# Optimization experiments

Hardware: AMD Instinct MI355X
Metric: run time of the kernel (lower is better)

## Reference

```python
import jax, jax.numpy as jnp
import numpy as np

B, C, H, W = 4, 128, 64, 64


def setup_inputs() -> dict:
    key = jax.random.key(0)
    ks = jax.random.split(key, 7)
    s = 1.0 / np.sqrt(C)
    return {
        "x": jax.random.normal(ks[0], (B, C, H, W), dtype=jnp.float32),
        "Wq": jax.random.normal(ks[1], (C, C), dtype=jnp.float32) * s,
        "bq": jnp.zeros((C,), dtype=jnp.float32),
        "Wk": jax.random.normal(ks[2], (C, C), dtype=jnp.float32) * s,
        "bk": jnp.zeros((C,), dtype=jnp.float32),
        "Wv": jax.random.normal(ks[3], (C, C), dtype=jnp.float32) * s,
        "bv": jnp.zeros((C,), dtype=jnp.float32),
    }


def reference(x, Wq, bq, Wk, bk, Wv, bv):
    b, c, h, w = x.shape
    n = h * w
    scale = c ** (-0.5)
    # tokens: [B, N, C]
    xt = x.reshape(b, c, n).transpose(0, 2, 1)
    # 1x1 convs == per-token channel GEMMs (out[c'] = sum_c W[c',c] x[c] + b[c'])
    q = jnp.einsum("bnc,dc->bnd", xt, Wq) + bq  # [B, N, C]
    k = jnp.einsum("bnc,dc->bnd", xt, Wk) + bk  # [B, N, C]
    v = jnp.einsum("bnc,dc->bnd", xt, Wv) + bv  # [B, N, C]
    scores = jnp.einsum("bic,bjc->bij", q, k) * scale  # [B, N, N]
    attn = jax.nn.softmax(scores, axis=-1)
    out = jnp.einsum("bij,bjc->bic", attn, v)  # [B, N, C]
    return out.transpose(0, 2, 1).reshape(b, c, h, w)
```

## Files before the change

### kernel.cpp

```cpp
#include <hip/hip_runtime.h>
#include <hip/hip_bf16.h>


#define BATCH 4
#define CH    128
#define NTOK  4096
#define TK    64
#define SCALE 0.08838834764831845f
#define LOG2E 1.4426950408889634f
#define MFIX  16.0f

typedef __attribute__((ext_vector_type(8)))  short short8;
typedef __attribute__((ext_vector_type(4)))  float f32x4;
typedef __attribute__((ext_vector_type(16))) float f32x16;

static __device__ __forceinline__ unsigned short f2bf(float f) {
    __hip_bfloat16 h = (__hip_bfloat16)f;
    return *(const unsigned short*)&h;
}

static __device__ __forceinline__ unsigned cvt_pk_bf16(float lo, float hi) {
    unsigned r;
    asm("v_cvt_pk_bf16_f32 %0, %1, %2" : "=v"(r) : "v"(lo), "v"(hi));
    return r;
}

__global__ __launch_bounds__(256) void convert_w_kernel(
    const float* __restrict__ Wq, const float* __restrict__ Wk,
    const float* __restrict__ Wv, unsigned short* __restrict__ wb)
{
    const int idx = (blockIdx.x * 256 + threadIdx.x) * 4;
    const float* srcs[3] = {Wq, Wk, Wv};
    #pragma unroll
    for (int m = 0; m < 3; ++m) {
        float4 v = *(const float4*)(srcs[m] + idx);
        unsigned short o[4] = {f2bf(v.x), f2bf(v.y), f2bf(v.z), f2bf(v.w)};
        *(uint2*)(wb + (size_t)m * CH * CH + idx) = *(const uint2*)o;
    }
}

__global__ __launch_bounds__(256) void proj_mfma_kernel(
    const float* __restrict__ x,
    const unsigned short* __restrict__ wb_all,
    const float* __restrict__ bq, const float* __restrict__ bk,
    const float* __restrict__ bv,
    unsigned short* __restrict__ q_ws, unsigned short* __restrict__ k_ws,
    unsigned short* __restrict__ vt_ws)
{
    __shared__ __align__(16) unsigned short XsT[64 * CH];

    const int t    = threadIdx.x;
    const int w    = t >> 6;
    const int lane = t & 63;
    const int quad = lane >> 4;
    const int c16  = lane & 15;
    const int n0   = blockIdx.x * 64;
    const int b    = blockIdx.y;
    const int z    = blockIdx.z;
    const float* xb = x + (size_t)b * CH * NTOK;

    {
        const int tok = lane;
        #pragma unroll
        for (int cc = 0; cc < 4; ++cc) {
            const int cb = 32 * w + 8 * cc;
            unsigned short tmp[8];
            #pragma unroll
            for (int j = 0; j < 8; ++j)
                tmp[j] = f2bf(xb[(size_t)(cb + j) * NTOK + n0 + tok]);
            const int phys = ((cb >> 3) ^ (tok & 15));
            *(short8*)&XsT[tok * CH + phys * 8] = *(const short8*)tmp;
        }
    }
    __syncthreads();

    if (z < 2) {
        const unsigned short* wm = wb_all + (size_t)z * CH * CH;
        const float* bias = (z == 0) ? bq : bk;
        unsigned short* dst = (z == 0) ? q_ws : k_ws;
        const float mul = (z == 0) ? (SCALE * LOG2E) : 1.0f;

        short8 xa[4];
        #pragma unroll
        for (int ks = 0; ks < 4; ++ks)
            xa[ks] = *(const short8*)&XsT[(16 * w + c16) * CH + (((4 * ks + quad) ^ c16) << 3)];

        #pragma unroll
        for (int nt = 0; nt < 8; ++nt) {
            f32x4 a = (f32x4){0.f, 0.f, 0.f, 0.f};
            const unsigned short* wr = wm + (16 * nt + c16) * CH;
            #pragma unroll
            for (int ks = 0; ks < 4; ++ks) {
                const short8 bf = *(const short8*)(wr + 32 * ks + 8 * quad);
                a = __builtin_amdgcn_mfma_f32_16x16x32_bf16(xa[ks], bf, a, 0, 0, 0);
            }
            const float bvv = bias[16 * nt + c16];
            #pragma unroll
            for (int r = 0; r < 4; ++r) {
                const int n = n0 + 16 * w + quad * 4 + r;
                dst[((size_t)b * NTOK + n) * CH + 16 * nt + c16] =
                    f2bf((a[r] + bvv) * mul);
            }
        }
    } else {
        const unsigned short* wvb = wb_all + (size_t)2 * CH * CH;
        short8 wva[2][4];
        float  bvv[2][4];
        #pragma unroll
        for (int mt = 0; mt < 2; ++mt) {
            const int crow16 = 16 * (2 * w + mt);
            #pragma unroll
            for (int ks = 0; ks < 4; ++ks)
                wva[mt][ks] = *(const short8*)&wvb[(crow16 + c16) * CH + 32 * ks + 8 * quad];
            #pragma unroll
            for (int r = 0; r < 4; ++r)
                bvv[mt][r] = bv[crow16 + quad * 4 + r];
        }
        #pragma unroll
        for (int nt = 0; nt < 4; ++nt) {
            short8 xbf[4];
            #pragma unroll
            for (int ks = 0; ks < 4; ++ks)
                xbf[ks] = *(const short8*)&XsT[(16 * nt + c16) * CH + (((4 * ks + quad) ^ c16) << 3)];
            #pragma unroll
            for (int mt = 0; mt < 2; ++mt) {
                f32x4 acc = (f32x4){0.f, 0.f, 0.f, 0.f};
                #pragma unroll
                for (int ks = 0; ks < 4; ++ks)
                    acc = __builtin_amdgcn_mfma_f32_16x16x32_bf16(wva[mt][ks], xbf[ks], acc, 0, 0, 0);
                #pragma unroll
                for (int r = 0; r < 4; ++r) {
                    const int crow = 16 * (2 * w + mt) + quad * 4 + r;
                    vt_ws[((size_t)b * CH + crow) * NTOK + n0 + 16 * nt + c16] =
                        f2bf(acc[r] + bvv[mt][r]);
                }
            }
        }
    }
}

template <int SPLIT>
__global__ __launch_bounds__(256, 2) void flash_attn_mfma(
    const unsigned short* __restrict__ q_ws,
    const unsigned short* __restrict__ k_ws,
    const unsigned short* __restrict__ vt_ws,
    float* __restrict__ out,
    float* __restrict__ Op, float* __restrict__ l_p)
{
    __shared__ __align__(16) unsigned short KsU[2][TK * CH];
    __shared__ __align__(16) unsigned short VtU[2][CH * TK];

    const int t    = threadIdx.x;
    const int w    = t >> 6;
    const int lane = t & 63;
    const int half = lane >> 5;
    const int l32  = lane & 31;
    const int jc   = blockIdx.y;
    const int b    = blockIdx.z;
    const int n0   = blockIdx.x * 128;
    const int jbeg = jc * (NTOK / SPLIT);
    constexpr int NT = (NTOK / SPLIT) / TK;

    const unsigned short* kg = k_ws  + (size_t)b * NTOK * CH;
    const unsigned short* vg = vt_ws + (size_t)b * CH * NTOK;

    short8 qa[8];
    {
        const unsigned short* qrow =
            q_ws + ((size_t)b * NTOK + n0 + 32 * w + l32) * CH;
        #pragma unroll
        for (int ks = 0; ks < 8; ++ks)
            qa[ks] = *(const short8*)(qrow + ks * 16 + half * 8);
    }

    f32x16 Oa[4];
    #pragma unroll
    for (int ct = 0; ct < 4; ++ct) Oa[ct] = (f32x16)(0.0f);
    float lsum = 0.f;

    const int krl = lane >> 4, ku = lane & 15;
    const int vcl = lane >> 3, vu = lane & 7;

    auto STAGE = [&](int buf, int jj) {
        #pragma unroll
        for (int ci = 0; ci < 4; ++ci) {
            const int row = 16 * w + 4 * ci + krl;
            const int g   = ku ^ (row & 15);
            const unsigned short* src = kg + (size_t)(jj + row) * CH + g * 8;
            __builtin_amdgcn_global_load_lds(
                (const __attribute__((address_space(1))) void*)src,
                (__attribute__((address_space(3))) void*)&KsU[buf][(16 * w + 4 * ci) * CH],
                16, 0, 0);
        }
        #pragma unroll
        for (int ci = 0; ci < 4; ++ci) {
            const int c = 32 * w + 8 * ci + vcl;
            const int g = vu ^ (c & 7);
            const unsigned short* src = vg + (size_t)c * NTOK + jj + g * 8;
            __builtin_amdgcn_global_load_lds(
                (const __attribute__((address_space(1))) void*)src,
                (__attribute__((address_space(3))) void*)&VtU[buf][(32 * w + 8 * ci) * TK],
                16, 0, 0);
        }
    };

    STAGE(0, jbeg);

    int j0 = jbeg;
    for (int tt = 0; tt < NT; ++tt, j0 += TK) {
        const int cur = tt & 1;
        if (tt + 1 < NT) {
            STAGE(cur ^ 1, j0 + TK);
            asm volatile("s_waitcnt vmcnt(8)" ::: "memory");
        } else {
            asm volatile("s_waitcnt vmcnt(0)" ::: "memory");
        }
        __builtin_amdgcn_sched_barrier(0);
        __builtin_amdgcn_s_barrier();
        __builtin_amdgcn_sched_barrier(0);

        const unsigned short* Kc = &KsU[cur][0];
        const unsigned short* Vc = &VtU[cur][0];

        f32x16 s[2];
        s[0] = (f32x16)(-MFIX);
        s[1] = (f32x16)(-MFIX);
        #pragma unroll
        for (int ks = 0; ks < 8; ++ks) {
            const int ph = (2 * ks + half) ^ (l32 & 15);
            const short8 kf0 = *(const short8*)&Kc[l32 * CH + ph * 8];
            const short8 kf1 = *(const short8*)&Kc[(32 + l32) * CH + ph * 8];
            s[0] = __builtin_amdgcn_mfma_f32_32x32x16_bf16(kf0, qa[ks], s[0], 0, 0, 0);
            s[1] = __builtin_amdgcn_mfma_f32_32x32x16_bf16(kf1, qa[ks], s[1], 0, 0, 0);
        }

        short8 pb[4];
        #pragma unroll
        for (int kt = 0; kt < 2; ++kt) {
            float p[16];
            #pragma unroll
            for (int r = 0; r < 16; ++r) p[r] = exp2f(s[kt][r]);
            float a0 = 0.f, a1 = 0.f, a2 = 0.f, a3 = 0.f;
            #pragma unroll
            for (int r = 0; r < 4; ++r) {
                a0 += p[r]; a1 += p[4 + r]; a2 += p[8 + r]; a3 += p[12 + r];
            }
            lsum += (a0 + a1) + (a2 + a3);
            unsigned wd[8];
            #pragma unroll
            for (int i = 0; i < 8; ++i) wd[i] = cvt_pk_bf16(p[2 * i], p[2 * i + 1]);
            auto r02 = __builtin_amdgcn_permlane32_swap(wd[0], wd[2], false, false);
            auto r13 = __builtin_amdgcn_permlane32_swap(wd[1], wd[3], false, false);
            auto r46 = __builtin_amdgcn_permlane32_swap(wd[4], wd[6], false, false);
            auto r57 = __builtin_amdgcn_permlane32_swap(wd[5], wd[7], false, false);
            union { unsigned u[4]; short8 s8; } f0, f1;
            f0.u[0] = r02[0]; f0.u[1] = r13[0]; f0.u[2] = r02[1]; f0.u[3] = r13[1];
            f1.u[0] = r46[0]; f1.u[1] = r57[0]; f1.u[2] = r46[1]; f1.u[3] = r57[1];
            pb[2 * kt + 0] = f0.s8;
            pb[2 * kt + 1] = f1.s8;
        }

        #pragma unroll
        for (int ks2 = 0; ks2 < 4; ++ks2) {
            #pragma unroll
            for (int ct = 0; ct < 4; ++ct) {
                const int ch = 32 * ct + l32;
                const int ph = (2 * ks2 + half) ^ (ch & 7);
                const short8 vf = *(const short8*)&Vc[ch * TK + ph * 8];
                Oa[ct] = __builtin_amdgcn_mfma_f32_32x32x16_bf16(vf, pb[ks2], Oa[ct], 0, 0, 0);
            }
        }
        __builtin_amdgcn_sched_barrier(0);
        __builtin_amdgcn_s_barrier();
        __builtin_amdgcn_sched_barrier(0);
    }

    const float lt = lsum + __shfl_xor(lsum, 32);
    const int n = n0 + 32 * w + l32;

    if constexpr (SPLIT == 1) {
        const float inv = 1.0f / lt;
        #pragma unroll
        for (int ct = 0; ct < 4; ++ct) {
            #pragma unroll
            for (int r = 0; r < 16; ++r) {
                const int c = 32 * ct + (r & 3) + 8 * (r >> 2) + 4 * half;
                out[((size_t)b * CH + c) * NTOK + n] = Oa[ct][r] * inv;
            }
        }
    } else {
        const size_t chunk = (size_t)(b * SPLIT + jc);
        #pragma unroll
        for (int ct = 0; ct < 4; ++ct) {
            #pragma unroll
            for (int r = 0; r < 16; ++r) {
                const int c = 32 * ct + (r & 3) + 8 * (r >> 2) + 4 * half;
                Op[(chunk * CH + c) * NTOK + n] = Oa[ct][r];
            }
        }
        if (half == 0) l_p[chunk * NTOK + n] = lt;
    }
}

template <int SPLIT>
__global__ __launch_bounds__(256) void combine_kernel(
    const float* __restrict__ Op, const float* __restrict__ l_p,
    float* __restrict__ out)
{
    const int b = blockIdx.y;
    const size_t idx = ((size_t)blockIdx.x * 256 + threadIdx.x) * 4;
    const int c = (int)(idx >> 12);
    const int n = (int)(idx & (NTOK - 1));
    float4 acc = make_float4(0.f, 0.f, 0.f, 0.f);
    float4 den = make_float4(0.f, 0.f, 0.f, 0.f);
    #pragma unroll
    for (int j = 0; j < SPLIT; ++j) {
        const size_t chunk = (size_t)(b * SPLIT + j);
        const float4 o = *(const float4*)&Op[(chunk * CH + c) * NTOK + n];
        const float4 d = *(const float4*)&l_p[chunk * NTOK + n];
        acc.x += o.x; acc.y += o.y; acc.z += o.z; acc.w += o.w;
        den.x += d.x; den.y += d.y; den.z += d.z; den.w += d.w;
    }
    float4 r;
    r.x = acc.x / den.x; r.y = acc.y / den.y;
    r.z = acc.z / den.z; r.w = acc.w / den.w;
    *(float4*)&out[((size_t)b * CH * NTOK) + idx] = r;
}

extern "C" void kernel_launch(void* const* d_in, const int* in_sizes, int n_in,
                              void* d_out, int out_size, void* d_ws, size_t ws_size,
                              hipStream_t stream) {
    const float* x  = (const float*)d_in[0];
    const float* Wq = (const float*)d_in[1];
    const float* bq = (const float*)d_in[2];
    const float* Wk = (const float*)d_in[3];
    const float* bk = (const float*)d_in[4];
    const float* Wv = (const float*)d_in[5];
    const float* bv = (const float*)d_in[6];
    float* out = (float*)d_out;

    const size_t QKV = (size_t)BATCH * NTOK * CH;
    unsigned short* q_ws  = (unsigned short*)d_ws;
    unsigned short* k_ws  = q_ws + QKV;
    unsigned short* vt_ws = k_ws + QKV;
    unsigned short* wb    = vt_ws + QKV;
    float* Op = (float*)(wb + 3 * CH * CH);

    const size_t baseBytes = 3 * QKV * 2 + 3 * CH * CH * 2;
    auto needBytes = [&](size_t S) {
        return baseBytes + S * BATCH * NTOK * (size_t)(CH * 4 + 4);
    };

    convert_w_kernel<<<CH * CH / (256 * 4), 256, 0, stream>>>(Wq, Wk, Wv, wb);

    dim3 gp(NTOK / 64, BATCH, 3);
    proj_mfma_kernel<<<gp, 256, 0, stream>>>(x, wb, bq, bk, bv, q_ws, k_ws, vt_ws);

    dim3 gc(CH * NTOK / 1024, BATCH);
    if (ws_size >= needBytes(4)) {
        float* l_p = Op + (size_t)4 * BATCH * NTOK * CH;
        dim3 ga(NTOK / 128, 4, BATCH);
        flash_attn_mfma<4><<<ga, 256, 0, stream>>>(q_ws, k_ws, vt_ws, out, Op, l_p);
        combine_kernel<4><<<gc, 256, 0, stream>>>(Op, l_p, out);
    } else if (ws_size >= needBytes(2)) {
        float* l_p = Op + (size_t)2 * BATCH * NTOK * CH;
        dim3 ga(NTOK / 128, 2, BATCH);
        flash_attn_mfma<2><<<ga, 256, 0, stream>>>(q_ws, k_ws, vt_ws, out, Op, l_p);
        combine_kernel<2><<<gc, 256, 0, stream>>>(Op, l_p, out);
    } else {
        dim3 ga(NTOK / 128, 1, BATCH);
        flash_attn_mfma<1><<<ga, 256, 0, stream>>>(q_ws, k_ws, vt_ws, out,
                                                   nullptr, nullptr);
    }
}
```

Measured before the change: 132.1 us.

## Stage projection stores via LDS, register-stage V tiles, split attention 8-way

The projection kernel now writes its bf16 Q/K and V^T results into a padded shared-memory tile first, then issues coalesced 16-byte global stores instead of scattered 2-byte ones. In the flash-attention kernel, V is loaded into registers and written to a single shared buffer, while K keeps its double-buffered direct-to-LDS DMA. The loop is unrolled by two with explicit wait/barrier points, and launch bounds are raised to 3 blocks per CU now that LDS use is smaller. The host also prefers an 8-way key split when workspace allows, at the cost of more partial-output traffic in the combine step.

```diff
diff --git a/kernel.cpp b/kernel.cpp
--- a/kernel.cpp
+++ b/kernel.cpp
@@ -48,6 +48,7 @@
     unsigned short* __restrict__ vt_ws)
 {
     __shared__ __align__(16) unsigned short XsT[64 * CH];
+    __shared__ __align__(16) unsigned short Ep[128 * 72];
 
     const int t    = threadIdx.x;
     const int w    = t >> 6;
@@ -97,10 +98,17 @@
             const float bvv = bias[16 * nt + c16];
             #pragma unroll
             for (int r = 0; r < 4; ++r) {
-                const int n = n0 + 16 * w + quad * 4 + r;
-                dst[((size_t)b * NTOK + n) * CH + 16 * nt + c16] =
-                    f2bf((a[r] + bvv) * mul);
-            }
+                const int tok = 16 * w + quad * 4 + r;
+                Ep[tok * 136 + 16 * nt + c16] = f2bf((a[r] + bvv) * mul);
+            }
+        }
+        __syncthreads();
+        #pragma unroll
+        for (int p = 0; p < 4; ++p) {
+            const int tok = p * 16 + (t >> 4);
+            const int u   = t & 15;
+            const uint4 v = *(const uint4*)&Ep[tok * 136 + u * 8];
+            *(uint4*)&dst[((size_t)b * NTOK + n0 + tok) * CH + u * 8] = v;
         }
     } else {
         const unsigned short* wvb = wb_all + (size_t)2 * CH * CH;
@@ -131,16 +139,23 @@
                 #pragma unroll
                 for (int r = 0; r < 4; ++r) {
                     const int crow = 16 * (2 * w + mt) + quad * 4 + r;
-                    vt_ws[((size_t)b * CH + crow) * NTOK + n0 + 16 * nt + c16] =
-                        f2bf(acc[r] + bvv[mt][r]);
+                    Ep[crow * 72 + 16 * nt + c16] = f2bf(acc[r] + bvv[mt][r]);
                 }
             }
         }
+        __syncthreads();
+        #pragma unroll
+        for (int p = 0; p < 4; ++p) {
+            const int c = p * 32 + (t >> 3);
+            const int u = t & 7;
+            const uint4 v = *(const uint4*)&Ep[c * 72 + u * 8];
+            *(uint4*)&vt_ws[((size_t)b * CH + c) * NTOK + n0 + u * 8] = v;
+        }
     }
 }
 
 template <int SPLIT>
-__global__ __launch_bounds__(256, 2) void flash_attn_mfma(
+__global__ __launch_bounds__(256, 3) void flash_attn_mfma(
     const unsigned short* __restrict__ q_ws,
     const unsigned short* __restrict__ k_ws,
     const unsigned short* __restrict__ vt_ws,
@@ -148,7 +163,7 @@
     float* __restrict__ Op, float* __restrict__ l_p)
 {
     __shared__ __align__(16) unsigned short KsU[2][TK * CH];
-    __shared__ __align__(16) unsigned short VtU[2][CH * TK];
+    __shared__ __align__(16) unsigned short VtU[CH * TK];
 
     const int t    = threadIdx.x;
     const int w    = t >> 6;
@@ -160,6 +175,7 @@
     const int n0   = blockIdx.x * 128;
     const int jbeg = jc * (NTOK / SPLIT);
     constexpr int NT = (NTOK / SPLIT) / TK;
+    static_assert(NT % 2 == 0, "NT must be even");
 
     const unsigned short* kg = k_ws  + (size_t)b * NTOK * CH;
     const unsigned short* vg = vt_ws + (size_t)b * CH * NTOK;
@@ -181,7 +197,7 @@
     const int krl = lane >> 4, ku = lane & 15;
     const int vcl = lane >> 3, vu = lane & 7;
 
-    auto STAGE = [&](int buf, int jj) {
+    auto K_DMA = [&](int buf, int jj) {
         #pragma unroll
         for (int ci = 0; ci < 4; ++ci) {
             const int row = 16 * w + 4 * ci + krl;
@@ -192,36 +208,22 @@
                 (__attribute__((address_space(3))) void*)&KsU[buf][(16 * w + 4 * ci) * CH],
                 16, 0, 0);
         }
+    };
+    auto V_LOAD = [&](int jj, uint4* vr) {
         #pragma unroll
         for (int ci = 0; ci < 4; ++ci) {
             const int c = 32 * w + 8 * ci + vcl;
             const int g = vu ^ (c & 7);
-            const unsigned short* src = vg + (size_t)c * NTOK + jj + g * 8;
-            __builtin_amdgcn_global_load_lds(
-                (const __attribute__((address_space(1))) void*)src,
-                (__attribute__((address_space(3))) void*)&VtU[buf][(32 * w + 8 * ci) * TK],
-                16, 0, 0);
+            vr[ci] = *(const uint4*)(vg + (size_t)c * NTOK + jj + g * 8);
         }
     };
-
-    STAGE(0, jbeg);
-
-    int j0 = jbeg;
-    for (int tt = 0; tt < NT; ++tt, j0 += TK) {
-        const int cur = tt & 1;
-        if (tt + 1 < NT) {
-            STAGE(cur ^ 1, j0 + TK);
-            asm volatile("s_waitcnt vmcnt(8)" ::: "memory");
-        } else {
-            asm volatile("s_waitcnt vmcnt(0)" ::: "memory");
-        }
-        __builtin_amdgcn_sched_barrier(0);
-        __builtin_amdgcn_s_barrier();
-        __builtin_amdgcn_sched_barrier(0);
-
-        const unsigned short* Kc = &KsU[cur][0];
-        const unsigned short* Vc = &VtU[cur][0];
-
+    auto V_WRITE = [&](const uint4* vr) {
+        #pragma unroll
+        for (int ci = 0; ci < 4; ++ci)
+            *(uint4*)((char*)&VtU[(32 * w + 8 * ci) * TK] + lane * 16) = vr[ci];
+    };
+
+    auto COMPUTE = [&](const unsigned short* Kc) {
         f32x16 s[2];
         s[0] = (f32x16)(-MFIX);
         s[1] = (f32x16)(-MFIX);
@@ -233,7 +235,6 @@
             s[0] = __builtin_amdgcn_mfma_f32_32x32x16_bf16(kf0, qa[ks], s[0], 0, 0, 0);
             s[1] = __builtin_amdgcn_mfma_f32_32x32x16_bf16(kf1, qa[ks], s[1], 0, 0, 0);
         }
-
         short8 pb[4];
         #pragma unroll
         for (int kt = 0; kt < 2; ++kt) {
@@ -259,20 +260,55 @@
             pb[2 * kt + 0] = f0.s8;
             pb[2 * kt + 1] = f1.s8;
         }
-
         #pragma unroll
         for (int ks2 = 0; ks2 < 4; ++ks2) {
             #pragma unroll
             for (int ct = 0; ct < 4; ++ct) {
                 const int ch = 32 * ct + l32;
                 const int ph = (2 * ks2 + half) ^ (ch & 7);
-                const short8 vf = *(const short8*)&Vc[ch * TK + ph * 8];
+                const short8 vf = *(const short8*)&VtU[ch * TK + ph * 8];
                 Oa[ct] = __builtin_amdgcn_mfma_f32_32x32x16_bf16(vf, pb[ks2], Oa[ct], 0, 0, 0);
             }
         }
+    };
+
+    uint4 vrA[4], vrB[4];
+    K_DMA(0, jbeg);
+    V_LOAD(jbeg, vrA);
+
+    int j0 = jbeg;
+    #pragma unroll 1
+    for (int tp = 0; tp < NT / 2; ++tp) {
+        asm volatile("s_waitcnt vmcnt(0)" ::: "memory");
         __builtin_amdgcn_sched_barrier(0);
         __builtin_amdgcn_s_barrier();
         __builtin_amdgcn_sched_barrier(0);
+        V_WRITE(vrA);
+        K_DMA(1, j0 + TK);
+        V_LOAD(j0 + TK, vrB);
+        asm volatile("s_waitcnt lgkmcnt(0)" ::: "memory");
+        __builtin_amdgcn_sched_barrier(0);
+        __builtin_amdgcn_s_barrier();
+        __builtin_amdgcn_sched_barrier(0);
+        COMPUTE(&KsU[0][0]);
+
+        const bool pf = (tp + 1 < NT / 2);
+        asm volatile("s_waitcnt vmcnt(0)" ::: "memory");
+        __builtin_amdgcn_sched_barrier(0);
+        __builtin_amdgcn_s_barrier();
+        __builtin_amdgcn_sched_barrier(0);
+        V_WRITE(vrB);
+        if (pf) {
+            K_DMA(0, j0 + 2 * TK);
+            V_LOAD(j0 + 2 * TK, vrA);
+        }
+        asm volatile("s_waitcnt lgkmcnt(0)" ::: "memory");
+        __builtin_amdgcn_sched_barrier(0);
+        __builtin_amdgcn_s_barrier();
+        __builtin_amdgcn_sched_barrier(0);
+        COMPUTE(&KsU[1][0]);
+
+        j0 += 2 * TK;
     }
 
     const float lt = lsum + __shfl_xor(lsum, 32);
@@ -357,16 +393,16 @@
     proj_mfma_kernel<<<gp, 256, 0, stream>>>(x, wb, bq, bk, bv, q_ws, k_ws, vt_ws);
 
     dim3 gc(CH * NTOK / 1024, BATCH);
-    if (ws_size >= needBytes(4)) {
+    if (ws_size >= needBytes(8)) {
+        float* l_p = Op + (size_t)8 * BATCH * NTOK * CH;
+        dim3 ga(NTOK / 128, 8, BATCH);
+        flash_attn_mfma<8><<<ga, 256, 0, stream>>>(q_ws, k_ws, vt_ws, out, Op, l_p);
+        combine_kernel<8><<<gc, 256, 0, stream>>>(Op, l_p, out);
+    } else if (ws_size >= needBytes(4)) {
         float* l_p = Op + (size_t)4 * BATCH * NTOK * CH;
         dim3 ga(NTOK / 128, 4, BATCH);
         flash_attn_mfma<4><<<ga, 256, 0, stream>>>(q_ws, k_ws, vt_ws, out, Op, l_p);
         combine_kernel<4><<<gc, 256, 0, stream>>>(Op, l_p, out);
-    } else if (ws_size >= needBytes(2)) {
-        float* l_p = Op + (size_t)2 * BATCH * NTOK * CH;
-        dim3 ga(NTOK / 128, 2, BATCH);
-        flash_attn_mfma<2><<<ga, 256, 0, stream>>>(q_ws, k_ws, vt_ws, out, Op, l_p);
-        combine_kernel<2><<<gc, 256, 0, stream>>>(Op, l_p, out);
     } else {
         dim3 ga(NTOK / 128, 1, BATCH);
         flash_attn_mfma<1><<<ga, 256, 0, stream>>>(q_ws, k_ws, vt_ws, out,
```

New measurement: 261.4 us. +97.9%, slower.
